# Kernel optimization log

Measured on AMD Instinct MI355X. Metric: run time of the kernel, lower is better.

## Reference

```python
import jax, jax.numpy as jnp
import numpy as np
from jax.ops import segment_sum

N_NODES = 100000
N_EDGES = 3200000
NUM_FEATURES = 128
HIDDEN = 64
NUM_CLASSES = 40


def setup_inputs() -> dict:
    key = jax.random.key(0)
    k1, k2, k3, k4, k5, k6 = jax.random.split(key, 6)
    x = jax.random.normal(k1, (N_NODES, NUM_FEATURES), dtype=jnp.float32)
    edge_index = jax.random.randint(k2, (2, N_EDGES), 0, N_NODES, dtype=jnp.int64)
    # GCNConv params (glorot-ish scale)
    W1 = jax.random.normal(k3, (NUM_FEATURES, HIDDEN), dtype=jnp.float32) / np.sqrt(NUM_FEATURES)
    b1 = jnp.zeros((HIDDEN,), dtype=jnp.float32)
    W2 = jax.random.normal(k4, (HIDDEN, NUM_CLASSES), dtype=jnp.float32) / np.sqrt(HIDDEN)
    b2 = jnp.zeros((NUM_CLASSES,), dtype=jnp.float32)
    return {"x": x, "edge_index": edge_index, "W1": W1, "b1": b1, "W2": W2, "b2": b2}


def _gcn_conv(x, row, col, norm, W, b, n_nodes):
    # PyG GCNConv: linear transform, then D^{-1/2} A D^{-1/2} aggregation, then bias
    h = x @ W                               # [N, out]
    msg = norm[:, None] * h[row]            # gather + scale, [E+N, out]
    out = segment_sum(msg, col, num_segments=n_nodes)  # scatter-add to destinations
    return out + b


def reference(x, edge_index, W1, b1, W2, b2):
    n = x.shape[0]
    self_loop = jnp.arange(n, dtype=edge_index.dtype)
    row = jnp.concatenate([edge_index[0], self_loop])  # sources (with self loops)
    col = jnp.concatenate([edge_index[1], self_loop])  # destinations
    w = jnp.ones(row.shape[0], dtype=x.dtype)          # edge_weight = None -> ones
    deg = segment_sum(w, col, num_segments=n)
    dinv = jnp.where(deg > 0, jax.lax.rsqrt(deg), 0.0)
    norm = dinv[row] * w * dinv[col]                   # symmetric normalization

    h = jax.nn.relu(_gcn_conv(x, row, col, norm, W1, b1, n))
    # F.dropout(training=self.training) -> identity in eval mode
    h = _gcn_conv(h, row, col, norm, W2, b2, n)
    return jax.nn.log_softmax(h, axis=1)
```

## Files before the change

kernel.cpp:

```cpp
#include <hip/hip_runtime.h>

#define F_IN  128
#define F_HID 64
#define F_OUT 40
#define BSZ   256
#define BSH   8
#define NB_MAX 512
#define CAP   12288

typedef __attribute__((ext_vector_type(8))) short v8s;
typedef __attribute__((ext_vector_type(4))) float v4f;
typedef __attribute__((ext_vector_type(4))) unsigned u4v;

static __device__ __forceinline__ unsigned pack_bf16(float a, float b) {
    unsigned ua = __float_as_uint(a);
    unsigned ub = __float_as_uint(b);
    ua = (ua + 0x7fffu + ((ua >> 16) & 1u)) >> 16;
    ub = (ub + 0x7fffu + ((ub >> 16) & 1u)) & 0xffff0000u;
    return ua | ub;
}
static __device__ __forceinline__ float bf_lo(unsigned u) { return __uint_as_float(u << 16); }
static __device__ __forceinline__ float bf_hi(unsigned u) { return __uint_as_float(u & 0xffff0000u); }

__global__ void k_partition(const int* __restrict__ row, const int* __restrict__ col,
                            int E, int nb, int* __restrict__ gcur,
                            unsigned* __restrict__ bbuf) {
    __shared__ int hist[NB_MAX];
    __shared__ int cur[NB_MAX];
    int t = threadIdx.x;
    for (int i = t; i < nb; i += 256) hist[i] = 0;
    __syncthreads();
    int chunk = (E + gridDim.x - 1) / gridDim.x;
    int e0 = blockIdx.x * chunk;
    int e1 = min(E, e0 + chunk);
    for (int e = e0 + t; e < e1; e += 256)
        atomicAdd(&hist[col[e] >> BSH], 1);
    __syncthreads();
    for (int i = t; i < nb; i += 256)
        cur[i] = i * CAP + atomicAdd(&gcur[i], hist[i]);
    __syncthreads();
    for (int e = e0 + t; e < e1; e += 256) {
        int c = col[e];
        int b = c >> BSH;
        int pos = atomicAdd(&cur[b], 1);
        if (pos < (b + 1) * CAP)
            bbuf[pos] = ((unsigned)row[e] << BSH) | (unsigned)(c & (BSZ - 1));
    }
}

__global__ void __launch_bounds__(1024)
k_csr(const unsigned* __restrict__ bbuf, const int* __restrict__ gcur,
      int* __restrict__ beg, int* __restrict__ deg, float* __restrict__ dinv,
      int* __restrict__ srow, int n) {
    __shared__ unsigned pay[CAP];
    __shared__ int cnt[BSZ];
    __shared__ int cur[BSZ];
    int b = blockIdx.x, t = threadIdx.x;
    int nE = min(gcur[b], CAP);
    int base = b * CAP;
    if (t < BSZ) cnt[t] = 0;
    __syncthreads();
    for (int i = t; i < nE; i += 1024) {
        unsigned u = bbuf[base + i];
        pay[i] = u;
        atomicAdd(&cnt[u & (BSZ - 1)], 1);
    }
    __syncthreads();
    if (t < BSZ) cur[t] = cnt[t];
    __syncthreads();
    for (int off = 1; off < BSZ; off <<= 1) {
        int add = (t < BSZ && t >= off) ? cur[t - off] : 0;
        __syncthreads();
        if (t < BSZ) cur[t] += add;
        __syncthreads();
    }
    int node0 = b * BSZ;
    if (t < BSZ) {
        int ex = cur[t] - cnt[t];
        int node = node0 + t;
        if (node < n) {
            beg[node] = base + ex;
            deg[node] = cnt[t];
            dinv[node] = rsqrtf((float)cnt[t] + 1.0f);
        }
        cur[t] = ex;
    }
    __syncthreads();
    for (int i = t; i < nE; i += 1024) {
        unsigned u = pay[i];
        int pos = atomicAdd(&cur[u & (BSZ - 1)], 1);
        srow[base + pos] = (int)(u >> BSH);
    }
}

__global__ void k_w1frag(const float* __restrict__ W1, unsigned* __restrict__ w1f,
                         unsigned* __restrict__ h1b, unsigned* __restrict__ h2b,
                         int* __restrict__ gcur, int n) {
    int gid = blockIdx.x * 256 + threadIdx.x;
    if (gid < 32) h1b[(size_t)n * 32 + gid] = 0u;
    if (gid < 32) h2b[(size_t)n * 32 + gid] = 0u;
    if (gid < NB_MAX) gcur[gid] = 0;
    if (gid >= 16 * 64) return;
    int f = gid >> 6, l = gid & 63;
    int j0 = f >> 2, ks = f & 3;
    int col = 16 * j0 + (l & 15);
    int kb = ks * 32 + ((l >> 4) << 3);
#pragma unroll
    for (int d = 0; d < 4; ++d) {
        float a = W1[(kb + 2 * d) * F_HID + col];
        float b = W1[(kb + 2 * d + 1) * F_HID + col];
        w1f[(size_t)gid * 4 + d] = pack_bf16(a, b);
    }
}

__global__ void k_lin1(const float* __restrict__ x, const unsigned* __restrict__ w1f,
                       const float* __restrict__ dinv, unsigned* __restrict__ h1b, int n) {
    int t = threadIdx.x;
    int l = t & 63, w = t >> 6;
    int node0 = blockIdx.x * 64 + w * 16;
    int arow = min(node0 + (l & 15), n - 1);
    const u4v* wf4 = (const u4v*)w1f;
    v8s bf[16];
#pragma unroll
    for (int f = 0; f < 16; ++f) {
        u4v u = wf4[f * 64 + l];
        bf[f] = *(v8s*)&u;
    }
    v8s af[4];
#pragma unroll
    for (int ks = 0; ks < 4; ++ks) {
        int kb = ks * 32 + ((l >> 4) << 3);
        const float4* xp = (const float4*)&x[(size_t)arow * F_IN + kb];
        float4 x0 = xp[0], x1 = xp[1];
        u4v uu = { pack_bf16(x0.x, x0.y), pack_bf16(x0.z, x0.w),
                   pack_bf16(x1.x, x1.y), pack_bf16(x1.z, x1.w) };
        af[ks] = *(v8s*)&uu;
    }
#pragma unroll
    for (int j0 = 0; j0 < 4; ++j0) {
        v4f acc = {0.f, 0.f, 0.f, 0.f};
#pragma unroll
        for (int ks = 0; ks < 4; ++ks)
            acc = __builtin_amdgcn_mfma_f32_16x16x32_bf16(af[ks], bf[j0 * 4 + ks], acc, 0, 0, 0);
#pragma unroll
        for (int i = 0; i < 4; ++i) {
            int node = node0 + ((l >> 4) << 2) + i;
            float s = acc[i] * dinv[min(node, n - 1)];
            float pr = __shfl_xor(s, 1);
            if (!(l & 1) && node < n)
                h1b[(size_t)node * 32 + 8 * j0 + ((l & 15) >> 1)] = pack_bf16(s, pr);
        }
    }
}

#define ISSUE1(i, u) { int rr = __shfl(r, (i) * 8 + g); u = h1q[(size_t)rr * 8 + c]; }
#define ISSUE2(i, u) { int rr = __shfl(r, (i) * 8 + g); u = h2q[(size_t)rr * 8 + c]; }
#define ACCUM(u) { a0 += bf_lo(u.x); a1 += bf_hi(u.x); \
                   a2 += bf_lo(u.y); a3 += bf_hi(u.y); \
                   a4 += bf_lo(u.z); a5 += bf_hi(u.z); \
                   a6 += bf_lo(u.w); a7 += bf_hi(u.w); }

__global__ void k_agg1(const u4v* __restrict__ h1q, const int* __restrict__ beg,
                       const int* __restrict__ deg, const int* __restrict__ srow,
                       const float* __restrict__ dinv, const float* __restrict__ b1,
                       const float* __restrict__ W2, unsigned* __restrict__ h2b, int n) {
    __shared__ float W2s[F_HID * F_OUT];
    __shared__ float b1s[F_HID];
    __shared__ float zrow[4][F_HID];
    int t = threadIdx.x;
    for (int i = t; i < F_HID * F_OUT; i += 256) W2s[i] = W2[i];
    if (t < F_HID) b1s[t] = b1[t];
    __syncthreads();
    int lane = t & 63, w = t >> 6;
    int g = lane >> 3, c = lane & 7;
    int node = blockIdx.x * 4 + w;
    if (node >= n) return;
    int bg = beg[node], cnt = deg[node];
    float a0=0.f,a1=0.f,a2=0.f,a3=0.f,a4=0.f,a5=0.f,a6=0.f,a7=0.f;
    for (int e0 = 0; e0 < cnt; e0 += 64) {
        int m = min(64, cnt - e0);
        int r = (lane < m) ? srow[bg + e0 + lane] : n;
        int iters = (m + 7) >> 3;
        u4v u0, u1, u2, u3;
        ISSUE1(0, u0) ISSUE1(1, u1) ISSUE1(2, u2) ISSUE1(3, u3)
        ACCUM(u0) ACCUM(u1) ACCUM(u2) ACCUM(u3)
        if (iters > 4) {
            ISSUE1(4, u0)
            if (iters > 5) ISSUE1(5, u1)
            if (iters > 6) ISSUE1(6, u2)
            if (iters > 7) ISSUE1(7, u3)
            ACCUM(u0)
            if (iters > 5) ACCUM(u1)
            if (iters > 6) ACCUM(u2)
            if (iters > 7) ACCUM(u3)
        }
    }
#pragma unroll
    for (int off = 8; off <= 32; off <<= 1) {
        a0 += __shfl_xor(a0, off); a1 += __shfl_xor(a1, off);
        a2 += __shfl_xor(a2, off); a3 += __shfl_xor(a3, off);
        a4 += __shfl_xor(a4, off); a5 += __shfl_xor(a5, off);
        a6 += __shfl_xor(a6, off); a7 += __shfl_xor(a7, off);
    }
    float dv = dinv[node];
    if (g == 0) {
        u4v us = h1q[(size_t)node * 8 + c];
        a0 += bf_lo(us.x); a1 += bf_hi(us.x);
        a2 += bf_lo(us.y); a3 += bf_hi(us.y);
        a4 += bf_lo(us.z); a5 += bf_hi(us.z);
        a6 += bf_lo(us.w); a7 += bf_hi(us.w);
        float z;
        z = fmaf(a0, dv, b1s[8*c+0]); zrow[w][8*c+0] = z > 0.f ? z : 0.f;
        z = fmaf(a1, dv, b1s[8*c+1]); zrow[w][8*c+1] = z > 0.f ? z : 0.f;
        z = fmaf(a2, dv, b1s[8*c+2]); zrow[w][8*c+2] = z > 0.f ? z : 0.f;
        z = fmaf(a3, dv, b1s[8*c+3]); zrow[w][8*c+3] = z > 0.f ? z : 0.f;
        z = fmaf(a4, dv, b1s[8*c+4]); zrow[w][8*c+4] = z > 0.f ? z : 0.f;
        z = fmaf(a5, dv, b1s[8*c+5]); zrow[w][8*c+5] = z > 0.f ? z : 0.f;
        z = fmaf(a6, dv, b1s[8*c+6]); zrow[w][8*c+6] = z > 0.f ? z : 0.f;
        z = fmaf(a7, dv, b1s[8*c+7]); zrow[w][8*c+7] = z > 0.f ? z : 0.f;
    }
    float s = 0.f;
    if (lane < F_OUT) {
#pragma unroll
        for (int k = 0; k < F_HID; ++k)
            s = fmaf(zrow[w][k], W2s[k * F_OUT + lane], s);
        s *= dv;
    }
    float partner = __shfl_xor(s, 1);
    if (lane < F_OUT && (lane & 1) == 0)
        h2b[(size_t)node * 32 + (lane >> 1)] = pack_bf16(s, partner);
}

__global__ void k_agg2(const u4v* __restrict__ h2q, const int* __restrict__ beg,
                       const int* __restrict__ deg, const int* __restrict__ srow,
                       const float* __restrict__ dinv, const float* __restrict__ b2,
                       float* __restrict__ out, int n) {
    int t = threadIdx.x, lane = t & 63, w = t >> 6;
    int g = lane >> 3, c = lane & 7;
    bool act = c < 5;
    int node = blockIdx.x * 4 + w;
    if (node >= n) return;
    int bg = beg[node], cnt = deg[node];
    float a0=0.f,a1=0.f,a2=0.f,a3=0.f,a4=0.f,a5=0.f,a6=0.f,a7=0.f;
    for (int e0 = 0; e0 < cnt; e0 += 64) {
        int m = min(64, cnt - e0);
        int r = (lane < m) ? srow[bg + e0 + lane] : n;
        int iters = (m + 7) >> 3;
        u4v u0, u1, u2, u3;
        ISSUE2(0, u0) ISSUE2(1, u1) ISSUE2(2, u2) ISSUE2(3, u3)
        ACCUM(u0) ACCUM(u1) ACCUM(u2) ACCUM(u3)
        if (iters > 4) {
            ISSUE2(4, u0)
            if (iters > 5) ISSUE2(5, u1)
            if (iters > 6) ISSUE2(6, u2)
            if (iters > 7) ISSUE2(7, u3)
            ACCUM(u0)
            if (iters > 5) ACCUM(u1)
            if (iters > 6) ACCUM(u2)
            if (iters > 7) ACCUM(u3)
        }
    }
#pragma unroll
    for (int off = 8; off <= 32; off <<= 1) {
        a0 += __shfl_xor(a0, off); a1 += __shfl_xor(a1, off);
        a2 += __shfl_xor(a2, off); a3 += __shfl_xor(a3, off);
        a4 += __shfl_xor(a4, off); a5 += __shfl_xor(a5, off);
        a6 += __shfl_xor(a6, off); a7 += __shfl_xor(a7, off);
    }
    float dv = dinv[node];
    float v0=-1e30f,v1=-1e30f,v2=-1e30f,v3=-1e30f,v4=-1e30f,v5=-1e30f,v6=-1e30f,v7=-1e30f;
    if (act) {
        u4v us = h2q[(size_t)node * 8 + c];
        v0 = fmaf(a0 + bf_lo(us.x), dv, b2[8*c+0]);
        v1 = fmaf(a1 + bf_hi(us.x), dv, b2[8*c+1]);
        v2 = fmaf(a2 + bf_lo(us.y), dv, b2[8*c+2]);
        v3 = fmaf(a3 + bf_hi(us.y), dv, b2[8*c+3]);
        v4 = fmaf(a4 + bf_lo(us.z), dv, b2[8*c+4]);
        v5 = fmaf(a5 + bf_hi(us.z), dv, b2[8*c+5]);
        v6 = fmaf(a6 + bf_lo(us.w), dv, b2[8*c+6]);
        v7 = fmaf(a7 + bf_hi(us.w), dv, b2[8*c+7]);
    }
    float mx = fmaxf(fmaxf(fmaxf(v0, v1), fmaxf(v2, v3)),
                     fmaxf(fmaxf(v4, v5), fmaxf(v6, v7)));
#pragma unroll
    for (int off = 1; off <= 4; off <<= 1) mx = fmaxf(mx, __shfl_xor(mx, off));
    float ex = 0.f;
    if (act)
        ex = expf(v0-mx)+expf(v1-mx)+expf(v2-mx)+expf(v3-mx)
           + expf(v4-mx)+expf(v5-mx)+expf(v6-mx)+expf(v7-mx);
#pragma unroll
    for (int off = 1; off <= 4; off <<= 1) ex += __shfl_xor(ex, off);
    float lg = logf(ex);
    if (g == 0 && act) {
        float4 o0, o1;
        o0.x = v0-mx-lg; o0.y = v1-mx-lg; o0.z = v2-mx-lg; o0.w = v3-mx-lg;
        o1.x = v4-mx-lg; o1.y = v5-mx-lg; o1.z = v6-mx-lg; o1.w = v7-mx-lg;
        float4* dst = reinterpret_cast<float4*>(&out[(size_t)node * F_OUT + 8 * c]);
        dst[0] = o0;
        dst[1] = o1;
    }
}

extern "C" void kernel_launch(void* const* d_in, const int* in_sizes, int n_in,
                              void* d_out, int out_size, void* d_ws, size_t ws_size,
                              hipStream_t stream) {
    const float* x  = (const float*)d_in[0];
    const int*   ei = (const int*)d_in[1];
    const float* W1 = (const float*)d_in[2];
    const float* b1 = (const float*)d_in[3];
    const float* W2 = (const float*)d_in[4];
    const float* b2 = (const float*)d_in[5];
    float* out = (float*)d_out;

    const int n = in_sizes[0] / F_IN;
    const int E = in_sizes[1] / 2;
    const int* row = ei;
    const int* col = ei + E;
    const int nb = (n + BSZ - 1) / BSZ;

    char* p = (char*)d_ws;
    float*    dinv = (float*)p;     p += (size_t)n * 4;
    int*      beg  = (int*)p;       p += (size_t)n * 4;
    int*      deg  = (int*)p;       p += (size_t)n * 4;
    int*      gcur = (int*)p;       p += NB_MAX * 4;
    unsigned* w1f  = (unsigned*)p;  p += 16 * 64 * 4 * 4;
    unsigned* bbuf = (unsigned*)p;  p += (size_t)nb * CAP * 4;
    int*      srow = (int*)p;       p += (size_t)nb * CAP * 4;
    unsigned* h1b  = (unsigned*)p;  p += (size_t)(n + 1) * 32 * 4;
    unsigned* h2b  = (unsigned*)p;  p += (size_t)(n + 1) * 32 * 4;

    k_w1frag<<<4, 256, 0, stream>>>(W1, w1f, h1b, h2b, gcur, n);
    k_partition<<<640, 256, 0, stream>>>(row, col, E, nb, gcur, bbuf);
    k_csr<<<nb, 1024, 0, stream>>>(bbuf, gcur, beg, deg, dinv, srow, n);
    k_lin1<<<(n + 63) / 64, 256, 0, stream>>>(x, w1f, dinv, h1b, n);
    k_agg1<<<(n + 3) / 4, 256, 0, stream>>>((const u4v*)h1b, beg, deg, srow, dinv, b1, W2, h2b, n);
    k_agg2<<<(n + 3) / 4, 256, 0, stream>>>((const u4v*)h2b, beg, deg, srow, dinv, b2, out, n);
}
```

Before: 253.8 us.

## Process two destination nodes per wavefront in both aggregation kernels

Each wavefront in k_agg1 and k_agg2 now aggregates two consecutive nodes, interleaving the neighbor gathers for both so more independent loads are in flight. The W2 staging and block setup are amortized over eight nodes per block instead of four, and the launch grids are halved. The trade-off is higher register pressure and wasted gather slots when the two nodes' degrees differ, since the loop runs to the larger count.

```diff
diff --git a/kernel.cpp b/kernel.cpp
--- a/kernel.cpp
+++ b/kernel.cpp
@@ -153,12 +153,11 @@
     }
 }
 
-#define ISSUE1(i, u) { int rr = __shfl(r, (i) * 8 + g); u = h1q[(size_t)rr * 8 + c]; }
-#define ISSUE2(i, u) { int rr = __shfl(r, (i) * 8 + g); u = h2q[(size_t)rr * 8 + c]; }
-#define ACCUM(u) { a0 += bf_lo(u.x); a1 += bf_hi(u.x); \
-                   a2 += bf_lo(u.y); a3 += bf_hi(u.y); \
-                   a4 += bf_lo(u.z); a5 += bf_hi(u.z); \
-                   a6 += bf_lo(u.w); a7 += bf_hi(u.w); }
+#define ISS(tq, rv, i, u) { int rr = __shfl(rv, (i) * 8 + g); u = tq[(size_t)rr * 8 + c]; }
+#define ACC(u, p0,p1,p2,p3,p4,p5,p6,p7) { \
+    p0 += bf_lo(u.x); p1 += bf_hi(u.x); p2 += bf_lo(u.y); p3 += bf_hi(u.y); \
+    p4 += bf_lo(u.z); p5 += bf_hi(u.z); p6 += bf_lo(u.w); p7 += bf_hi(u.w); }
+#define RED(p) { p += __shfl_xor(p, 8); p += __shfl_xor(p, 16); p += __shfl_xor(p, 32); }
 
 __global__ void k_agg1(const u4v* __restrict__ h1q, const int* __restrict__ beg,
                        const int* __restrict__ deg, const int* __restrict__ srow,
@@ -166,69 +165,89 @@
                        const float* __restrict__ W2, unsigned* __restrict__ h2b, int n) {
     __shared__ float W2s[F_HID * F_OUT];
     __shared__ float b1s[F_HID];
-    __shared__ float zrow[4][F_HID];
+    __shared__ float zrow[8][F_HID];
     int t = threadIdx.x;
     for (int i = t; i < F_HID * F_OUT; i += 256) W2s[i] = W2[i];
     if (t < F_HID) b1s[t] = b1[t];
     __syncthreads();
     int lane = t & 63, w = t >> 6;
     int g = lane >> 3, c = lane & 7;
-    int node = blockIdx.x * 4 + w;
-    if (node >= n) return;
-    int bg = beg[node], cnt = deg[node];
-    float a0=0.f,a1=0.f,a2=0.f,a3=0.f,a4=0.f,a5=0.f,a6=0.f,a7=0.f;
-    for (int e0 = 0; e0 < cnt; e0 += 64) {
-        int m = min(64, cnt - e0);
-        int r = (lane < m) ? srow[bg + e0 + lane] : n;
-        int iters = (m + 7) >> 3;
-        u4v u0, u1, u2, u3;
-        ISSUE1(0, u0) ISSUE1(1, u1) ISSUE1(2, u2) ISSUE1(3, u3)
-        ACCUM(u0) ACCUM(u1) ACCUM(u2) ACCUM(u3)
+    int nA = blockIdx.x * 8 + w * 2;
+    if (nA >= n) return;
+    int nB = nA + 1;
+    bool hasB = nB < n;
+    int bgA = beg[nA], cntA = deg[nA];
+    int bgB = hasB ? beg[nB] : 0, cntB = hasB ? deg[nB] : 0;
+    float a0=0,a1=0,a2=0,a3=0,a4=0,a5=0,a6=0,a7=0;
+    float b0=0,b1_=0,b2_=0,b3=0,b4=0,b5=0,b6=0,b7=0;
+    int cmax = max(cntA, cntB);
+    for (int e0 = 0; e0 < cmax; e0 += 64) {
+        int rA = (lane < cntA - e0) ? srow[bgA + e0 + lane] : n;
+        int rB = (lane < cntB - e0) ? srow[bgB + e0 + lane] : n;
+        int iters = (min(cmax - e0, 64) + 7) >> 3;
+        u4v uA0, uA1, uA2, uA3, uB0, uB1, uB2, uB3;
+        ISS(h1q, rA, 0, uA0) ISS(h1q, rB, 0, uB0)
+        ISS(h1q, rA, 1, uA1) ISS(h1q, rB, 1, uB1)
+        ISS(h1q, rA, 2, uA2) ISS(h1q, rB, 2, uB2)
+        ISS(h1q, rA, 3, uA3) ISS(h1q, rB, 3, uB3)
+        ACC(uA0, a0,a1,a2,a3,a4,a5,a6,a7) ACC(uB0, b0,b1_,b2_,b3,b4,b5,b6,b7)
+        ACC(uA1, a0,a1,a2,a3,a4,a5,a6,a7) ACC(uB1, b0,b1_,b2_,b3,b4,b5,b6,b7)
+        ACC(uA2, a0,a1,a2,a3,a4,a5,a6,a7) ACC(uB2, b0,b1_,b2_,b3,b4,b5,b6,b7)
+        ACC(uA3, a0,a1,a2,a3,a4,a5,a6,a7) ACC(uB3, b0,b1_,b2_,b3,b4,b5,b6,b7)
         if (iters > 4) {
-            ISSUE1(4, u0)
-            if (iters > 5) ISSUE1(5, u1)
-            if (iters > 6) ISSUE1(6, u2)
-            if (iters > 7) ISSUE1(7, u3)
-            ACCUM(u0)
-            if (iters > 5) ACCUM(u1)
-            if (iters > 6) ACCUM(u2)
-            if (iters > 7) ACCUM(u3)
-        }
-    }
-#pragma unroll
-    for (int off = 8; off <= 32; off <<= 1) {
-        a0 += __shfl_xor(a0, off); a1 += __shfl_xor(a1, off);
-        a2 += __shfl_xor(a2, off); a3 += __shfl_xor(a3, off);
-        a4 += __shfl_xor(a4, off); a5 += __shfl_xor(a5, off);
-        a6 += __shfl_xor(a6, off); a7 += __shfl_xor(a7, off);
-    }
-    float dv = dinv[node];
+            ISS(h1q, rA, 4, uA0) ISS(h1q, rB, 4, uB0)
+            if (iters > 5) { ISS(h1q, rA, 5, uA1) ISS(h1q, rB, 5, uB1) }
+            if (iters > 6) { ISS(h1q, rA, 6, uA2) ISS(h1q, rB, 6, uB2) }
+            if (iters > 7) { ISS(h1q, rA, 7, uA3) ISS(h1q, rB, 7, uB3) }
+            ACC(uA0, a0,a1,a2,a3,a4,a5,a6,a7) ACC(uB0, b0,b1_,b2_,b3,b4,b5,b6,b7)
+            if (iters > 5) { ACC(uA1, a0,a1,a2,a3,a4,a5,a6,a7) ACC(uB1, b0,b1_,b2_,b3,b4,b5,b6,b7) }
+            if (iters > 6) { ACC(uA2, a0,a1,a2,a3,a4,a5,a6,a7) ACC(uB2, b0,b1_,b2_,b3,b4,b5,b6,b7) }
+            if (iters > 7) { ACC(uA3, a0,a1,a2,a3,a4,a5,a6,a7) ACC(uB3, b0,b1_,b2_,b3,b4,b5,b6,b7) }
+        }
+    }
+    RED(a0) RED(a1) RED(a2) RED(a3) RED(a4) RED(a5) RED(a6) RED(a7)
+    RED(b0) RED(b1_) RED(b2_) RED(b3) RED(b4) RED(b5) RED(b6) RED(b7)
     if (g == 0) {
-        u4v us = h1q[(size_t)node * 8 + c];
-        a0 += bf_lo(us.x); a1 += bf_hi(us.x);
-        a2 += bf_lo(us.y); a3 += bf_hi(us.y);
-        a4 += bf_lo(us.z); a5 += bf_hi(us.z);
-        a6 += bf_lo(us.w); a7 += bf_hi(us.w);
+        u4v us = h1q[(size_t)nA * 8 + c];
+        float dv = dinv[nA];
         float z;
-        z = fmaf(a0, dv, b1s[8*c+0]); zrow[w][8*c+0] = z > 0.f ? z : 0.f;
-        z = fmaf(a1, dv, b1s[8*c+1]); zrow[w][8*c+1] = z > 0.f ? z : 0.f;
-        z = fmaf(a2, dv, b1s[8*c+2]); zrow[w][8*c+2] = z > 0.f ? z : 0.f;
-        z = fmaf(a3, dv, b1s[8*c+3]); zrow[w][8*c+3] = z > 0.f ? z : 0.f;
-        z = fmaf(a4, dv, b1s[8*c+4]); zrow[w][8*c+4] = z > 0.f ? z : 0.f;
-        z = fmaf(a5, dv, b1s[8*c+5]); zrow[w][8*c+5] = z > 0.f ? z : 0.f;
-        z = fmaf(a6, dv, b1s[8*c+6]); zrow[w][8*c+6] = z > 0.f ? z : 0.f;
-        z = fmaf(a7, dv, b1s[8*c+7]); zrow[w][8*c+7] = z > 0.f ? z : 0.f;
-    }
-    float s = 0.f;
+        z = fmaf(a0 + bf_lo(us.x), dv, b1s[8*c+0]); zrow[2*w][8*c+0] = z > 0.f ? z : 0.f;
+        z = fmaf(a1 + bf_hi(us.x), dv, b1s[8*c+1]); zrow[2*w][8*c+1] = z > 0.f ? z : 0.f;
+        z = fmaf(a2 + bf_lo(us.y), dv, b1s[8*c+2]); zrow[2*w][8*c+2] = z > 0.f ? z : 0.f;
+        z = fmaf(a3 + bf_hi(us.y), dv, b1s[8*c+3]); zrow[2*w][8*c+3] = z > 0.f ? z : 0.f;
+        z = fmaf(a4 + bf_lo(us.z), dv, b1s[8*c+4]); zrow[2*w][8*c+4] = z > 0.f ? z : 0.f;
+        z = fmaf(a5 + bf_hi(us.z), dv, b1s[8*c+5]); zrow[2*w][8*c+5] = z > 0.f ? z : 0.f;
+        z = fmaf(a6 + bf_lo(us.w), dv, b1s[8*c+6]); zrow[2*w][8*c+6] = z > 0.f ? z : 0.f;
+        z = fmaf(a7 + bf_hi(us.w), dv, b1s[8*c+7]); zrow[2*w][8*c+7] = z > 0.f ? z : 0.f;
+    } else if (g == 1 && hasB) {
+        u4v us = h1q[(size_t)nB * 8 + c];
+        float dv = dinv[nB];
+        float z;
+        z = fmaf(b0  + bf_lo(us.x), dv, b1s[8*c+0]); zrow[2*w+1][8*c+0] = z > 0.f ? z : 0.f;
+        z = fmaf(b1_ + bf_hi(us.x), dv, b1s[8*c+1]); zrow[2*w+1][8*c+1] = z > 0.f ? z : 0.f;
+        z = fmaf(b2_ + bf_lo(us.y), dv, b1s[8*c+2]); zrow[2*w+1][8*c+2] = z > 0.f ? z : 0.f;
+        z = fmaf(b3  + bf_hi(us.y), dv, b1s[8*c+3]); zrow[2*w+1][8*c+3] = z > 0.f ? z : 0.f;
+        z = fmaf(b4  + bf_lo(us.z), dv, b1s[8*c+4]); zrow[2*w+1][8*c+4] = z > 0.f ? z : 0.f;
+        z = fmaf(b5  + bf_hi(us.z), dv, b1s[8*c+5]); zrow[2*w+1][8*c+5] = z > 0.f ? z : 0.f;
+        z = fmaf(b6  + bf_lo(us.w), dv, b1s[8*c+6]); zrow[2*w+1][8*c+6] = z > 0.f ? z : 0.f;
+        z = fmaf(b7  + bf_hi(us.w), dv, b1s[8*c+7]); zrow[2*w+1][8*c+7] = z > 0.f ? z : 0.f;
+    }
+    float sA = 0.f, sB = 0.f;
     if (lane < F_OUT) {
 #pragma unroll
-        for (int k = 0; k < F_HID; ++k)
-            s = fmaf(zrow[w][k], W2s[k * F_OUT + lane], s);
-        s *= dv;
-    }
-    float partner = __shfl_xor(s, 1);
-    if (lane < F_OUT && (lane & 1) == 0)
-        h2b[(size_t)node * 32 + (lane >> 1)] = pack_bf16(s, partner);
+        for (int k = 0; k < F_HID; ++k) {
+            sA = fmaf(zrow[2*w][k],     W2s[k * F_OUT + lane], sA);
+            sB = fmaf(zrow[2*w+1][k],   W2s[k * F_OUT + lane], sB);
+        }
+        sA *= dinv[nA];
+        sB *= hasB ? dinv[nB] : 0.f;
+    }
+    float pA = __shfl_xor(sA, 1);
+    float pB = __shfl_xor(sB, 1);
+    if (lane < F_OUT && (lane & 1) == 0) {
+        h2b[(size_t)nA * 32 + (lane >> 1)] = pack_bf16(sA, pA);
+        if (hasB) h2b[(size_t)nB * 32 + (lane >> 1)] = pack_bf16(sB, pB);
+    }
 }
 
 __global__ void k_agg2(const u4v* __restrict__ h2q, const int* __restrict__ beg,
@@ -237,48 +256,61 @@
                        float* __restrict__ out, int n) {
     int t = threadIdx.x, lane = t & 63, w = t >> 6;
     int g = lane >> 3, c = lane & 7;
-    bool act = c < 5;
-    int node = blockIdx.x * 4 + w;
-    if (node >= n) return;
-    int bg = beg[node], cnt = deg[node];
-    float a0=0.f,a1=0.f,a2=0.f,a3=0.f,a4=0.f,a5=0.f,a6=0.f,a7=0.f;
-    for (int e0 = 0; e0 < cnt; e0 += 64) {
-        int m = min(64, cnt - e0);
-        int r = (lane < m) ? srow[bg + e0 + lane] : n;
-        int iters = (m + 7) >> 3;
-        u4v u0, u1, u2, u3;
-        ISSUE2(0, u0) ISSUE2(1, u1) ISSUE2(2, u2) ISSUE2(3, u3)
-        ACCUM(u0) ACCUM(u1) ACCUM(u2) ACCUM(u3)
+    int nA = blockIdx.x * 8 + w * 2;
+    if (nA >= n) return;
+    int nB = nA + 1;
+    bool hasB = nB < n;
+    int bgA = beg[nA], cntA = deg[nA];
+    int bgB = hasB ? beg[nB] : 0, cntB = hasB ? deg[nB] : 0;
+    float a0=0,a1=0,a2=0,a3=0,a4=0,a5=0,a6=0,a7=0;
+    float b0=0,b1_=0,b2_=0,b3=0,b4=0,b5=0,b6=0,b7=0;
+    int cmax = max(cntA, cntB);
+    for (int e0 = 0; e0 < cmax; e0 += 64) {
+        int rA = (lane < cntA - e0) ? srow[bgA + e0 + lane] : n;
+        int rB = (lane < cntB - e0) ? srow[bgB + e0 + lane] : n;
+        int iters = (min(cmax - e0, 64) + 7) >> 3;
+        u4v uA0, uA1, uA2, uA3, uB0, uB1, uB2, uB3;
+        ISS(h2q, rA, 0, uA0) ISS(h2q, rB, 0, uB0)
+        ISS(h2q, rA, 1, uA1) ISS(h2q, rB, 1, uB1)
+        ISS(h2q, rA, 2, uA2) ISS(h2q, rB, 2, uB2)
+        ISS(h2q, rA, 3, uA3) ISS(h2q, rB, 3, uB3)
+        ACC(uA0, a0,a1,a2,a3,a4,a5,a6,a7) ACC(uB0, b0,b1_,b2_,b3,b4,b5,b6,b7)
+        ACC(uA1, a0,a1,a2,a3,a4,a5,a6,a7) ACC(uB1, b0,b1_,b2_,b3,b4,b5,b6,b7)
+        ACC(uA2, a0,a1,a2,a3,a4,a5,a6,a7) ACC(uB2, b0,b1_,b2_,b3,b4,b5,b6,b7)
+        ACC(uA3, a0,a1,a2,a3,a4,a5,a6,a7) ACC(uB3, b0,b1_,b2_,b3,b4,b5,b6,b7)
         if (iters > 4) {
-            ISSUE2(4, u0)
-            if (iters > 5) ISSUE2(5, u1)
-            if (iters > 6) ISSUE2(6, u2)
-            if (iters > 7) ISSUE2(7, u3)
-            ACCUM(u0)
-            if (iters > 5) ACCUM(u1)
-            if (iters > 6) ACCUM(u2)
-            if (iters > 7) ACCUM(u3)
-        }
-    }
-#pragma unroll
-    for (int off = 8; off <= 32; off <<= 1) {
-        a0 += __shfl_xor(a0, off); a1 += __shfl_xor(a1, off);
-        a2 += __shfl_xor(a2, off); a3 += __shfl_xor(a3, off);
-        a4 += __shfl_xor(a4, off); a5 += __shfl_xor(a5, off);
-        a6 += __shfl_xor(a6, off); a7 += __shfl_xor(a7, off);
-    }
-    float dv = dinv[node];
+            ISS(h2q, rA, 4, uA0) ISS(h2q, rB, 4, uB0)
+            if (iters > 5) { ISS(h2q, rA, 5, uA1) ISS(h2q, rB, 5, uB1) }
+            if (iters > 6) { ISS(h2q, rA, 6, uA2) ISS(h2q, rB, 6, uB2) }
+            if (iters > 7) { ISS(h2q, rA, 7, uA3) ISS(h2q, rB, 7, uB3) }
+            ACC(uA0, a0,a1,a2,a3,a4,a5,a6,a7) ACC(uB0, b0,b1_,b2_,b3,b4,b5,b6,b7)
+            if (iters > 5) { ACC(uA1, a0,a1,a2,a3,a4,a5,a6,a7) ACC(uB1, b0,b1_,b2_,b3,b4,b5,b6,b7) }
+            if (iters > 6) { ACC(uA2, a0,a1,a2,a3,a4,a5,a6,a7) ACC(uB2, b0,b1_,b2_,b3,b4,b5,b6,b7) }
+            if (iters > 7) { ACC(uA3, a0,a1,a2,a3,a4,a5,a6,a7) ACC(uB3, b0,b1_,b2_,b3,b4,b5,b6,b7) }
+        }
+    }
+    RED(a0) RED(a1) RED(a2) RED(a3) RED(a4) RED(a5) RED(a6) RED(a7)
+    RED(b0) RED(b1_) RED(b2_) RED(b3) RED(b4) RED(b5) RED(b6) RED(b7)
+    bool isB = g >= 4;
+    int nd = isB ? nB : nA;
+    bool nodeOK = !isB || hasB;
+    bool act = (c < 5) && nodeOK;
     float v0=-1e30f,v1=-1e30f,v2=-1e30f,v3=-1e30f,v4=-1e30f,v5=-1e30f,v6=-1e30f,v7=-1e30f;
     if (act) {
-        u4v us = h2q[(size_t)node * 8 + c];
-        v0 = fmaf(a0 + bf_lo(us.x), dv, b2[8*c+0]);
-        v1 = fmaf(a1 + bf_hi(us.x), dv, b2[8*c+1]);
-        v2 = fmaf(a2 + bf_lo(us.y), dv, b2[8*c+2]);
-        v3 = fmaf(a3 + bf_hi(us.y), dv, b2[8*c+3]);
-        v4 = fmaf(a4 + bf_lo(us.z), dv, b2[8*c+4]);
-        v5 = fmaf(a5 + bf_hi(us.z), dv, b2[8*c+5]);
-        v6 = fmaf(a6 + bf_lo(us.w), dv, b2[8*c+6]);
-        v7 = fmaf(a7 + bf_hi(us.w), dv, b2[8*c+7]);
+        float dv = dinv[nd];
+        u4v us = h2q[(size_t)nd * 8 + c];
+        float e0 = isB ? b0  : a0, e1 = isB ? b1_ : a1;
+        float e2 = isB ? b2_ : a2, e3 = isB ? b3  : a3;
+        float e4 = isB ? b4  : a4, e5 = isB ? b5  : a5;
+        float e6 = isB ? b6  : a6, e7 = isB ? b7  : a7;
+        v0 = fmaf(e0 + bf_lo(us.x), dv, b2[8*c+0]);
+        v1 = fmaf(e1 + bf_hi(us.x), dv, b2[8*c+1]);
+        v2 = fmaf(e2 + bf_lo(us.y), dv, b2[8*c+2]);
+        v3 = fmaf(e3 + bf_hi(us.y), dv, b2[8*c+3]);
+        v4 = fmaf(e4 + bf_lo(us.z), dv, b2[8*c+4]);
+        v5 = fmaf(e5 + bf_hi(us.z), dv, b2[8*c+5]);
+        v6 = fmaf(e6 + bf_lo(us.w), dv, b2[8*c+6]);
+        v7 = fmaf(e7 + bf_hi(us.w), dv, b2[8*c+7]);
     }
     float mx = fmaxf(fmaxf(fmaxf(v0, v1), fmaxf(v2, v3)),
                      fmaxf(fmaxf(v4, v5), fmaxf(v6, v7)));
@@ -291,11 +323,11 @@
 #pragma unroll
     for (int off = 1; off <= 4; off <<= 1) ex += __shfl_xor(ex, off);
     float lg = logf(ex);
-    if (g == 0 && act) {
+    if (act && (g == 0 || g == 4)) {
         float4 o0, o1;
         o0.x = v0-mx-lg; o0.y = v1-mx-lg; o0.z = v2-mx-lg; o0.w = v3-mx-lg;
         o1.x = v4-mx-lg; o1.y = v5-mx-lg; o1.z = v6-mx-lg; o1.w = v7-mx-lg;
-        float4* dst = reinterpret_cast<float4*>(&out[(size_t)node * F_OUT + 8 * c]);
+        float4* dst = reinterpret_cast<float4*>(&out[(size_t)nd * F_OUT + 8 * c]);
         dst[0] = o0;
         dst[1] = o1;
     }
@@ -333,6 +365,6 @@
     k_partition<<<640, 256, 0, stream>>>(row, col, E, nb, gcur, bbuf);
     k_csr<<<nb, 1024, 0, stream>>>(bbuf, gcur, beg, deg, dinv, srow, n);
     k_lin1<<<(n + 63) / 64, 256, 0, stream>>>(x, w1f, dinv, h1b, n);
-    k_agg1<<<(n + 3) / 4, 256, 0, stream>>>((const u4v*)h1b, beg, deg, srow, dinv, b1, W2, h2b, n);
-    k_agg2<<<(n + 3) / 4, 256, 0, stream>>>((const u4v*)h2b, beg, deg, srow, dinv, b2, out, n);
-}
+    k_agg1<<<(n + 7) / 8, 256, 0, stream>>>((const u4v*)h1b, beg, deg, srow, dinv, b1, W2, h2b, n);
+    k_agg2<<<(n + 7) / 8, 256, 0, stream>>>((const u4v*)h2b, beg, deg, srow, dinv, b2, out, n);
+}
```

New measurement: 457.0 us. 80.0% more time.

## Process two nodes per wavefront in both aggregation kernels using half-wave gathers

Applied to the files above, without the earlier changes.

Each 64-lane wavefront now aggregates two destination nodes, one per 32-lane half, in both aggregation kernels. Each half covers up to 32 edges per chunk with 4 edge groups of 8 lanes. Average degree is about 33, so the old one-node-per-wave layout left many lanes idle. Packing two nodes per wave is meant to raise lane utilisation and halve the number of blocks launched. The cost is that each half runs for the larger of the two node degrees, which can cause divergence-driven waste.

```diff
diff --git a/kernel.cpp b/kernel.cpp
--- a/kernel.cpp
+++ b/kernel.cpp
@@ -153,12 +153,10 @@
     }
 }
 
-#define ISSUE1(i, u) { int rr = __shfl(r, (i) * 8 + g); u = h1q[(size_t)rr * 8 + c]; }
-#define ISSUE2(i, u) { int rr = __shfl(r, (i) * 8 + g); u = h2q[(size_t)rr * 8 + c]; }
-#define ACCUM(u) { a0 += bf_lo(u.x); a1 += bf_hi(u.x); \
-                   a2 += bf_lo(u.y); a3 += bf_hi(u.y); \
-                   a4 += bf_lo(u.z); a5 += bf_hi(u.z); \
-                   a6 += bf_lo(u.w); a7 += bf_hi(u.w); }
+#define ISS(tq, i, u) { int rr = __shfl(r, hb + (i) * 4 + gg); u = tq[(size_t)rr * 8 + c]; }
+#define ACC8(u) { a0 += bf_lo(u.x); a1 += bf_hi(u.x); a2 += bf_lo(u.y); a3 += bf_hi(u.y); \
+                  a4 += bf_lo(u.z); a5 += bf_hi(u.z); a6 += bf_lo(u.w); a7 += bf_hi(u.w); }
+#define RED2(p) { p += __shfl_xor(p, 8); p += __shfl_xor(p, 16); }
 
 __global__ void k_agg1(const u4v* __restrict__ h1q, const int* __restrict__ beg,
                        const int* __restrict__ deg, const int* __restrict__ srow,
@@ -166,69 +164,75 @@
                        const float* __restrict__ W2, unsigned* __restrict__ h2b, int n) {
     __shared__ float W2s[F_HID * F_OUT];
     __shared__ float b1s[F_HID];
-    __shared__ float zrow[4][F_HID];
+    __shared__ float zrow[8][F_HID];
     int t = threadIdx.x;
     for (int i = t; i < F_HID * F_OUT; i += 256) W2s[i] = W2[i];
     if (t < F_HID) b1s[t] = b1[t];
     __syncthreads();
     int lane = t & 63, w = t >> 6;
-    int g = lane >> 3, c = lane & 7;
-    int node = blockIdx.x * 4 + w;
-    if (node >= n) return;
-    int bg = beg[node], cnt = deg[node];
-    float a0=0.f,a1=0.f,a2=0.f,a3=0.f,a4=0.f,a5=0.f,a6=0.f,a7=0.f;
-    for (int e0 = 0; e0 < cnt; e0 += 64) {
-        int m = min(64, cnt - e0);
-        int r = (lane < m) ? srow[bg + e0 + lane] : n;
-        int iters = (m + 7) >> 3;
+    int h = lane >> 5, l5 = lane & 31;
+    int gg = (lane >> 3) & 3, c = lane & 7;
+    int hb = h << 5;
+    int nA = blockIdx.x * 8 + w * 2;
+    if (nA >= n) return;
+    int nB = nA + 1;
+    bool hasB = nB < n;
+    int nd = h ? nB : nA;
+    bool ok = (h == 0) || hasB;
+    int bg = ok ? beg[nd] : 0;
+    int cnt = ok ? deg[nd] : 0;
+    int cmax = max(__shfl(cnt, 0), __shfl(cnt, 32));
+    float a0=0,a1=0,a2=0,a3=0,a4=0,a5=0,a6=0,a7=0;
+    for (int e0 = 0; e0 < cmax; e0 += 32) {
+        int r = (l5 < cnt - e0) ? srow[bg + e0 + l5] : n;
+        int iters = (min(cmax - e0, 32) + 3) >> 2;
         u4v u0, u1, u2, u3;
-        ISSUE1(0, u0) ISSUE1(1, u1) ISSUE1(2, u2) ISSUE1(3, u3)
-        ACCUM(u0) ACCUM(u1) ACCUM(u2) ACCUM(u3)
+        ISS(h1q, 0, u0) ISS(h1q, 1, u1) ISS(h1q, 2, u2) ISS(h1q, 3, u3)
+        ACC8(u0)
+        if (iters > 1) ACC8(u1)
+        if (iters > 2) ACC8(u2)
+        if (iters > 3) ACC8(u3)
         if (iters > 4) {
-            ISSUE1(4, u0)
-            if (iters > 5) ISSUE1(5, u1)
-            if (iters > 6) ISSUE1(6, u2)
-            if (iters > 7) ISSUE1(7, u3)
-            ACCUM(u0)
-            if (iters > 5) ACCUM(u1)
-            if (iters > 6) ACCUM(u2)
-            if (iters > 7) ACCUM(u3)
-        }
-    }
-#pragma unroll
-    for (int off = 8; off <= 32; off <<= 1) {
-        a0 += __shfl_xor(a0, off); a1 += __shfl_xor(a1, off);
-        a2 += __shfl_xor(a2, off); a3 += __shfl_xor(a3, off);
-        a4 += __shfl_xor(a4, off); a5 += __shfl_xor(a5, off);
-        a6 += __shfl_xor(a6, off); a7 += __shfl_xor(a7, off);
-    }
-    float dv = dinv[node];
-    if (g == 0) {
-        u4v us = h1q[(size_t)node * 8 + c];
-        a0 += bf_lo(us.x); a1 += bf_hi(us.x);
-        a2 += bf_lo(us.y); a3 += bf_hi(us.y);
-        a4 += bf_lo(us.z); a5 += bf_hi(us.z);
-        a6 += bf_lo(us.w); a7 += bf_hi(us.w);
+            ISS(h1q, 4, u0)
+            if (iters > 5) ISS(h1q, 5, u1)
+            if (iters > 6) ISS(h1q, 6, u2)
+            if (iters > 7) ISS(h1q, 7, u3)
+            ACC8(u0)
+            if (iters > 5) ACC8(u1)
+            if (iters > 6) ACC8(u2)
+            if (iters > 7) ACC8(u3)
+        }
+    }
+    RED2(a0) RED2(a1) RED2(a2) RED2(a3) RED2(a4) RED2(a5) RED2(a6) RED2(a7)
+    if (gg == 0 && ok) {
+        u4v us = h1q[(size_t)nd * 8 + c];
+        float dv = dinv[nd];
         float z;
-        z = fmaf(a0, dv, b1s[8*c+0]); zrow[w][8*c+0] = z > 0.f ? z : 0.f;
-        z = fmaf(a1, dv, b1s[8*c+1]); zrow[w][8*c+1] = z > 0.f ? z : 0.f;
-        z = fmaf(a2, dv, b1s[8*c+2]); zrow[w][8*c+2] = z > 0.f ? z : 0.f;
-        z = fmaf(a3, dv, b1s[8*c+3]); zrow[w][8*c+3] = z > 0.f ? z : 0.f;
-        z = fmaf(a4, dv, b1s[8*c+4]); zrow[w][8*c+4] = z > 0.f ? z : 0.f;
-        z = fmaf(a5, dv, b1s[8*c+5]); zrow[w][8*c+5] = z > 0.f ? z : 0.f;
-        z = fmaf(a6, dv, b1s[8*c+6]); zrow[w][8*c+6] = z > 0.f ? z : 0.f;
-        z = fmaf(a7, dv, b1s[8*c+7]); zrow[w][8*c+7] = z > 0.f ? z : 0.f;
-    }
-    float s = 0.f;
+        z = fmaf(a0 + bf_lo(us.x), dv, b1s[8*c+0]); zrow[2*w+h][8*c+0] = z > 0.f ? z : 0.f;
+        z = fmaf(a1 + bf_hi(us.x), dv, b1s[8*c+1]); zrow[2*w+h][8*c+1] = z > 0.f ? z : 0.f;
+        z = fmaf(a2 + bf_lo(us.y), dv, b1s[8*c+2]); zrow[2*w+h][8*c+2] = z > 0.f ? z : 0.f;
+        z = fmaf(a3 + bf_hi(us.y), dv, b1s[8*c+3]); zrow[2*w+h][8*c+3] = z > 0.f ? z : 0.f;
+        z = fmaf(a4 + bf_lo(us.z), dv, b1s[8*c+4]); zrow[2*w+h][8*c+4] = z > 0.f ? z : 0.f;
+        z = fmaf(a5 + bf_hi(us.z), dv, b1s[8*c+5]); zrow[2*w+h][8*c+5] = z > 0.f ? z : 0.f;
+        z = fmaf(a6 + bf_lo(us.w), dv, b1s[8*c+6]); zrow[2*w+h][8*c+6] = z > 0.f ? z : 0.f;
+        z = fmaf(a7 + bf_hi(us.w), dv, b1s[8*c+7]); zrow[2*w+h][8*c+7] = z > 0.f ? z : 0.f;
+    }
+    float sA = 0.f, sB = 0.f;
     if (lane < F_OUT) {
 #pragma unroll
-        for (int k = 0; k < F_HID; ++k)
-            s = fmaf(zrow[w][k], W2s[k * F_OUT + lane], s);
-        s *= dv;
-    }
-    float partner = __shfl_xor(s, 1);
-    if (lane < F_OUT && (lane & 1) == 0)
-        h2b[(size_t)node * 32 + (lane >> 1)] = pack_bf16(s, partner);
+        for (int k = 0; k < F_HID; ++k) {
+            sA = fmaf(zrow[2*w][k],   W2s[k * F_OUT + lane], sA);
+            sB = fmaf(zrow[2*w+1][k], W2s[k * F_OUT + lane], sB);
+        }
+        sA *= dinv[nA];
+        sB *= hasB ? dinv[nB] : 0.f;
+    }
+    float pA = __shfl_xor(sA, 1);
+    float pB = __shfl_xor(sB, 1);
+    if (lane < F_OUT && (lane & 1) == 0) {
+        h2b[(size_t)nA * 32 + (lane >> 1)] = pack_bf16(sA, pA);
+        if (hasB) h2b[(size_t)nB * 32 + (lane >> 1)] = pack_bf16(sB, pB);
+    }
 }
 
 __global__ void k_agg2(const u4v* __restrict__ h2q, const int* __restrict__ beg,
@@ -236,41 +240,45 @@
                        const float* __restrict__ dinv, const float* __restrict__ b2,
                        float* __restrict__ out, int n) {
     int t = threadIdx.x, lane = t & 63, w = t >> 6;
-    int g = lane >> 3, c = lane & 7;
-    bool act = c < 5;
-    int node = blockIdx.x * 4 + w;
-    if (node >= n) return;
-    int bg = beg[node], cnt = deg[node];
-    float a0=0.f,a1=0.f,a2=0.f,a3=0.f,a4=0.f,a5=0.f,a6=0.f,a7=0.f;
-    for (int e0 = 0; e0 < cnt; e0 += 64) {
-        int m = min(64, cnt - e0);
-        int r = (lane < m) ? srow[bg + e0 + lane] : n;
-        int iters = (m + 7) >> 3;
+    int h = lane >> 5, l5 = lane & 31;
+    int gg = (lane >> 3) & 3, c = lane & 7;
+    int hb = h << 5;
+    int nA = blockIdx.x * 8 + w * 2;
+    if (nA >= n) return;
+    int nB = nA + 1;
+    bool hasB = nB < n;
+    int nd = h ? nB : nA;
+    bool ok = (h == 0) || hasB;
+    int bg = ok ? beg[nd] : 0;
+    int cnt = ok ? deg[nd] : 0;
+    int cmax = max(__shfl(cnt, 0), __shfl(cnt, 32));
+    float a0=0,a1=0,a2=0,a3=0,a4=0,a5=0,a6=0,a7=0;
+    for (int e0 = 0; e0 < cmax; e0 += 32) {
+        int r = (l5 < cnt - e0) ? srow[bg + e0 + l5] : n;
+        int iters = (min(cmax - e0, 32) + 3) >> 2;
         u4v u0, u1, u2, u3;
-        ISSUE2(0, u0) ISSUE2(1, u1) ISSUE2(2, u2) ISSUE2(3, u3)
-        ACCUM(u0) ACCUM(u1) ACCUM(u2) ACCUM(u3)
+        ISS(h2q, 0, u0) ISS(h2q, 1, u1) ISS(h2q, 2, u2) ISS(h2q, 3, u3)
+        ACC8(u0)
+        if (iters > 1) ACC8(u1)
+        if (iters > 2) ACC8(u2)
+        if (iters > 3) ACC8(u3)
         if (iters > 4) {
-            ISSUE2(4, u0)
-            if (iters > 5) ISSUE2(5, u1)
-            if (iters > 6) ISSUE2(6, u2)
-            if (iters > 7) ISSUE2(7, u3)
-            ACCUM(u0)
-            if (iters > 5) ACCUM(u1)
-            if (iters > 6) ACCUM(u2)
-            if (iters > 7) ACCUM(u3)
-        }
-    }
-#pragma unroll
-    for (int off = 8; off <= 32; off <<= 1) {
-        a0 += __shfl_xor(a0, off); a1 += __shfl_xor(a1, off);
-        a2 += __shfl_xor(a2, off); a3 += __shfl_xor(a3, off);
-        a4 += __shfl_xor(a4, off); a5 += __shfl_xor(a5, off);
-        a6 += __shfl_xor(a6, off); a7 += __shfl_xor(a7, off);
-    }
-    float dv = dinv[node];
+            ISS(h2q, 4, u0)
+            if (iters > 5) ISS(h2q, 5, u1)
+            if (iters > 6) ISS(h2q, 6, u2)
+            if (iters > 7) ISS(h2q, 7, u3)
+            ACC8(u0)
+            if (iters > 5) ACC8(u1)
+            if (iters > 6) ACC8(u2)
+            if (iters > 7) ACC8(u3)
+        }
+    }
+    RED2(a0) RED2(a1) RED2(a2) RED2(a3) RED2(a4) RED2(a5) RED2(a6) RED2(a7)
+    bool act = (c < 5) && ok;
     float v0=-1e30f,v1=-1e30f,v2=-1e30f,v3=-1e30f,v4=-1e30f,v5=-1e30f,v6=-1e30f,v7=-1e30f;
     if (act) {
-        u4v us = h2q[(size_t)node * 8 + c];
+        float dv = dinv[nd];
+        u4v us = h2q[(size_t)nd * 8 + c];
         v0 = fmaf(a0 + bf_lo(us.x), dv, b2[8*c+0]);
         v1 = fmaf(a1 + bf_hi(us.x), dv, b2[8*c+1]);
         v2 = fmaf(a2 + bf_lo(us.y), dv, b2[8*c+2]);
@@ -291,11 +299,11 @@
 #pragma unroll
     for (int off = 1; off <= 4; off <<= 1) ex += __shfl_xor(ex, off);
     float lg = logf(ex);
-    if (g == 0 && act) {
+    if (act && gg == 0) {
         float4 o0, o1;
         o0.x = v0-mx-lg; o0.y = v1-mx-lg; o0.z = v2-mx-lg; o0.w = v3-mx-lg;
         o1.x = v4-mx-lg; o1.y = v5-mx-lg; o1.z = v6-mx-lg; o1.w = v7-mx-lg;
-        float4* dst = reinterpret_cast<float4*>(&out[(size_t)node * F_OUT + 8 * c]);
+        float4* dst = reinterpret_cast<float4*>(&out[(size_t)nd * F_OUT + 8 * c]);
         dst[0] = o0;
         dst[1] = o1;
     }
@@ -333,6 +341,6 @@
     k_partition<<<640, 256, 0, stream>>>(row, col, E, nb, gcur, bbuf);
     k_csr<<<nb, 1024, 0, stream>>>(bbuf, gcur, beg, deg, dinv, srow, n);
     k_lin1<<<(n + 63) / 64, 256, 0, stream>>>(x, w1f, dinv, h1b, n);
-    k_agg1<<<(n + 3) / 4, 256, 0, stream>>>((const u4v*)h1b, beg, deg, srow, dinv, b1, W2, h2b, n);
-    k_agg2<<<(n + 3) / 4, 256, 0, stream>>>((const u4v*)h2b, beg, deg, srow, dinv, b2, out, n);
-}
+    k_agg1<<<(n + 7) / 8, 256, 0, stream>>>((const u4v*)h1b, beg, deg, srow, dinv, b1, W2, h2b, n);
+    k_agg2<<<(n + 7) / 8, 256, 0, stream>>>((const u4v*)h2b, beg, deg, srow, dinv, b2, out, n);
+}
```

Result: slower. 442.8 us (+74.4%).
